# Kernel optimization log

Hardware: AMD Instinct MI355X
Metric: run time of the kernel (lower is better)

## Reference

```python
import jax, jax.numpy as jnp
import numpy as np

ALPHA = 0.2          # LeakyReLU negative slope
NEG = -9e15          # mask fill value, as in pyGAT GraphAttentionLayer
N, NIN, NHID, NOUT = 4096, 64, 32, 64
NHEADS, D_INT = 8, 32
H_INT = max(1, int(NHEADS * 0.25))   # 2 intent heads
H_SP = NHEADS - H_INT                # 6 spatial heads


def setup_inputs() -> dict:
    key = jax.random.key(0)
    ks = jax.random.split(key, 10)
    x = jax.random.normal(ks[0], (N, NIN), dtype=jnp.float32)
    adj = (jax.random.uniform(ks[1], (N, N)) < 0.01).astype(jnp.float32)
    adj = jnp.clip(adj + jnp.eye(N, dtype=jnp.float32), 0.0, 1.0)
    intent_embeds = jax.random.normal(ks[2], (N, D_INT), dtype=jnp.float32)
    # learned params (xavier-ish scale)
    def xav(k, shape):
        fan = shape[-2] if len(shape) > 1 else shape[-1]
        return jax.random.normal(k, shape, dtype=jnp.float32) / np.sqrt(fan)
    W_sp = xav(ks[3], (H_SP, NIN, NHID))       # spatial head projections
    a_sp = xav(ks[4], (H_SP, 2 * NHID))        # spatial attention vectors
    W_int = xav(ks[5], (H_INT, NIN, NHID))     # intent head projections
    a_int = xav(ks[6], (H_INT, 2 * D_INT))     # intent attention vectors (over intent embeds)
    W_out = xav(ks[7], (NHID * NHEADS, NOUT))  # output GAT layer
    a_out = xav(ks[8], (2 * NOUT,))
    return {"x": x, "adj": adj, "intent_embeds": intent_embeds,
            "W_sp": W_sp, "a_sp": a_sp, "W_int": W_int, "a_int": a_int,
            "W_out": W_out, "a_out": a_out}


def _masked_attend(e, mask, Wh):
    # e: [H,N,N] raw scores, mask: [1,N,N] bool, Wh: [H,N,F]
    att = jax.nn.softmax(jnp.where(mask, e, NEG), axis=-1)
    return jnp.einsum('hij,hjf->hif', att, Wh)


def reference(x, adj, intent_embeds, W_sp, a_sp, W_int, a_int, W_out, a_out):
    mask = (adj > 0)[None]                                   # [1,N,N]
    # ---- spatial heads (standard GAT, batched over heads) ----
    Wh_s = jnp.einsum('nf,hfo->hno', x, W_sp)                # [Hs,N,nhid]
    f1 = jnp.einsum('hno,ho->hn', Wh_s, a_sp[:, :NHID])
    f2 = jnp.einsum('hno,ho->hn', Wh_s, a_sp[:, NHID:])
    e_s = jax.nn.leaky_relu(f1[:, :, None] + f2[:, None, :], ALPHA)
    h_s = jax.nn.elu(_masked_attend(e_s, mask, Wh_s))        # concat=True -> elu
    # ---- intent heads: scores from intent embeddings, values from Wh ----
    Wh_i = jnp.einsum('nf,hfo->hno', x, W_int)               # [Hi,N,nhid]
    g1 = jnp.einsum('nd,hd->hn', intent_embeds, a_int[:, :D_INT])
    g2 = jnp.einsum('nd,hd->hn', intent_embeds, a_int[:, D_INT:])
    e_i = jax.nn.leaky_relu(g1[:, :, None] + g2[:, None, :], ALPHA)
    h_i = jax.nn.elu(_masked_attend(e_i, mask, Wh_i))        # [Hi,N,nhid]
    # ---- concat heads along feature dim: [N, nheads*nhid] ----
    h = jnp.concatenate([h_s, h_i], axis=0).transpose(1, 0, 2).reshape(N, -1)
    # ---- output attention layer (concat=False: no elu) ----
    Who = h @ W_out                                          # [N,nout]
    o1 = Who @ a_out[:NOUT]
    o2 = Who @ a_out[NOUT:]
    e_o = jax.nn.leaky_relu(o1[:, None] + o2[None, :], ALPHA)
    att_o = jax.nn.softmax(jnp.where(mask[0], e_o, NEG), axis=-1)
    out = att_o @ Who
    return jnp.tanh(out)
```

## Files before the change

### kernel.cpp

```cpp
#include <hip/hip_runtime.h>

#define N      4096
#define NIN    64
#define NHID   32
#define NOUT   64
#define NHEADS 8
#define H_SP   6
#define D_INT  32
#define MAXDEG 128
#define NPB    4
#define ROWS   8
#define WPAD   (MAXDEG + 4)
#define ALPHA  0.2f

__device__ __forceinline__ int mbcnt64(unsigned long long m) {
    return __builtin_amdgcn_mbcnt_hi((unsigned)(m >> 32),
           __builtin_amdgcn_mbcnt_lo((unsigned)m, 0u));
}

__global__ __launch_bounds__(256) void k_fused1(
    const float* __restrict__ x, const float* __restrict__ ie,
    const float4* __restrict__ adj4,
    const float* __restrict__ Wsp, const float* __restrict__ asp,
    const float* __restrict__ Wint, const float* __restrict__ aint,
    float* __restrict__ Wh_t, float* __restrict__ src, float* __restrict__ dst_t,
    int* __restrict__ col, int* __restrict__ deg)
{
    const int nb   = blockIdx.x * NPB;
    const int tid  = threadIdx.x;
    const int wv   = tid >> 6, lane = tid & 63;
    const int h    = tid >> 5, f    = tid & 31;

    __shared__ float xs_t[NIN][NPB];
    __shared__ float ies[NPB][D_INT];

    xs_t[tid & 63][tid >> 6] = x[nb * NIN + tid];
    if (tid < NPB * D_INT) ies[tid >> 5][tid & 31] = ie[nb * D_INT + tid];
    __syncthreads();

    const float* W = (h < H_SP) ? (Wsp + h * NIN * NHID)
                                : (Wint + (h - H_SP) * NIN * NHID);
    float acc[NPB] = {0.f, 0.f, 0.f, 0.f};
#pragma unroll
    for (int c = 0; c < NIN; ++c) {
        const float wval = W[c * NHID + f];
        const float4 xv  = *(const float4*)&xs_t[c][0];
        acc[0] += xv.x * wval; acc[1] += xv.y * wval;
        acc[2] += xv.z * wval; acc[3] += xv.w * wval;
    }
#pragma unroll
    for (int m = 0; m < NPB; ++m)
        Wh_t[(size_t)(nb + m) * 256 + tid] = acc[m];

    const float a1v = (h < H_SP) ? asp[h * 64 + f]      : aint[(h - H_SP) * 64 + f];
    const float a2v = (h < H_SP) ? asp[h * 64 + 32 + f] : aint[(h - H_SP) * 64 + 32 + f];
#pragma unroll
    for (int m = 0; m < NPB; ++m) {
        const float b = (h < H_SP) ? acc[m] : ies[m][f];
        float s1 = b * a1v, s2 = b * a2v;
#pragma unroll
        for (int mm = 16; mm >= 1; mm >>= 1) {
            s1 += __shfl_xor(s1, mm);
            s2 += __shfl_xor(s2, mm);
        }
        if (f == 0) { src[h * N + nb + m] = s1; dst_t[(nb + m) * 8 + h] = s2; }
    }

    const int r = nb + wv;
    const float4* row = adj4 + (size_t)r * (N / 4);
    int cnt = 0;
#pragma unroll 4
    for (int t = 0; t < 16; ++t) {
        float4 v = row[t * 64 + lane];
        unsigned long long bx = __ballot(v.x > 0.f);
        unsigned long long by = __ballot(v.y > 0.f);
        unsigned long long bz = __ballot(v.z > 0.f);
        unsigned long long bw = __ballot(v.w > 0.f);
        const int tx = __popcll(bx), ty = __popcll(by);
        const int tz = __popcll(bz), tw = __popcll(bw);
        const int idx0 = (t * 64 + lane) * 4;
        const int px = cnt + mbcnt64(bx);
        const int py = cnt + tx + mbcnt64(by);
        const int pz = cnt + tx + ty + mbcnt64(bz);
        const int pw = cnt + tx + ty + tz + mbcnt64(bw);
        if (v.x > 0.f && px < MAXDEG) col[r * MAXDEG + px] = idx0;
        if (v.y > 0.f && py < MAXDEG) col[r * MAXDEG + py] = idx0 + 1;
        if (v.z > 0.f && pz < MAXDEG) col[r * MAXDEG + pz] = idx0 + 2;
        if (v.w > 0.f && pw < MAXDEG) col[r * MAXDEG + pw] = idx0 + 3;
        cnt += tx + ty + tz + tw;
    }
    if (lane == 0) deg[r] = (cnt < MAXDEG) ? cnt : MAXDEG;
}

__global__ __launch_bounds__(512, 4) void k_attn1who(
    const int* __restrict__ col, const int* __restrict__ deg,
    const float* __restrict__ Wh_t, const float* __restrict__ src,
    const float* __restrict__ dst_t, const float* __restrict__ Wout,
    const float* __restrict__ aout,
    float* __restrict__ Who, float* __restrict__ o1, float* __restrict__ o2)
{
    const int r0   = blockIdx.x * ROWS;
    const int tid  = threadIdx.x;
    const int wv   = tid >> 6, lane = tid & 63;
    const int r    = r0 + wv;

    __shared__ __align__(16) int   cs[ROWS][MAXDEG];
    __shared__ __align__(16) float w_t[ROWS][NHEADS][WPAD];
    __shared__ __align__(16) float hs[ROWS][NHEADS * NHID];

    const int d  = deg[r];
    const int j0 = (lane < d)      ? col[r * MAXDEG + lane]      : 0;
    const int j1 = (lane + 64 < d) ? col[r * MAXDEG + 64 + lane] : 0;
    cs[wv][lane]      = j0;
    cs[wv][lane + 64] = j1;

    float sr[NHEADS];
#pragma unroll
    for (int h = 0; h < NHEADS; ++h) sr[h] = src[h * N + r];

    float dA[NHEADS] = {}, dB[NHEADS] = {};
    if (lane < d) {
        *(float4*)&dA[0] = *(const float4*)&dst_t[j0 * 8];
        *(float4*)&dA[4] = *(const float4*)&dst_t[j0 * 8 + 4];
    }
    if (lane + 64 < d) {
        *(float4*)&dB[0] = *(const float4*)&dst_t[j1 * 8];
        *(float4*)&dB[4] = *(const float4*)&dst_t[j1 * 8 + 4];
    }

#pragma unroll
    for (int h = 0; h < NHEADS; ++h) {
        float a = sr[h] + dA[h]; a = a > 0.f ? a : ALPHA * a;
        float b = sr[h] + dB[h]; b = b > 0.f ? b : ALPHA * b;
        w_t[wv][h][lane]      = (lane < d)      ? __expf(a) : 0.f;
        w_t[wv][h][lane + 64] = (lane + 64 < d) ? __expf(b) : 0.f;
    }

    const float* wrow = &w_t[wv][lane >> 3][0];
    const int*   csr_ = &cs[wv][0];
    float4 acc = make_float4(0.f, 0.f, 0.f, 0.f);
    float  ws  = 0.f;
    const int d4 = (d + 3) & ~3;
    for (int k = 0; k < d4; k += 4) {
        const int4   jj = *(const int4*)&csr_[k];
        const float4 wq = *(const float4*)&wrow[k];
        const float4 ga = *(const float4*)&Wh_t[(size_t)jj.x * 256 + 4 * lane];
        const float4 gb = *(const float4*)&Wh_t[(size_t)jj.y * 256 + 4 * lane];
        const float4 gc = *(const float4*)&Wh_t[(size_t)jj.z * 256 + 4 * lane];
        const float4 gd = *(const float4*)&Wh_t[(size_t)jj.w * 256 + 4 * lane];
        ws    += (wq.x + wq.y) + (wq.z + wq.w);
        acc.x += wq.x * ga.x + wq.y * gb.x + wq.z * gc.x + wq.w * gd.x;
        acc.y += wq.x * ga.y + wq.y * gb.y + wq.z * gc.y + wq.w * gd.y;
        acc.z += wq.x * ga.z + wq.y * gb.z + wq.z * gc.z + wq.w * gd.z;
        acc.w += wq.x * ga.w + wq.y * gb.w + wq.z * gc.w + wq.w * gd.w;
    }
    const float inv = 1.f / ws;
    acc.x *= inv; acc.y *= inv; acc.z *= inv; acc.w *= inv;
    acc.x = acc.x > 0.f ? acc.x : __expf(acc.x) - 1.f;
    acc.y = acc.y > 0.f ? acc.y : __expf(acc.y) - 1.f;
    acc.z = acc.z > 0.f ? acc.z : __expf(acc.z) - 1.f;
    acc.w = acc.w > 0.f ? acc.w : __expf(acc.w) - 1.f;
    *(float4*)&hs[wv][4 * lane] = acc;
    __syncthreads();

    float* part = &w_t[0][0][0];
    {
        float wreg[32];
#pragma unroll
        for (int cc = 0; cc < 32; ++cc)
            wreg[cc] = Wout[(wv * 32 + cc) * NOUT + lane];
#pragma unroll
        for (int m = 0; m < ROWS; ++m) {
            float a = 0.f;
#pragma unroll
            for (int cc = 0; cc < 32; cc += 4) {
                const float4 hv = *(const float4*)&hs[m][wv * 32 + cc];
                a += hv.x * wreg[cc]     + hv.y * wreg[cc + 1]
                   + hv.z * wreg[cc + 2] + hv.w * wreg[cc + 3];
            }
            part[(wv * ROWS + m) * NOUT + lane] = a;
        }
    }
    __syncthreads();

    float who = 0.f;
#pragma unroll
    for (int q = 0; q < 8; ++q) who += part[(q * ROWS + wv) * NOUT + lane];
    Who[(size_t)r * NOUT + lane] = who;
    float v1 = who * aout[lane];
    float v2 = who * aout[NOUT + lane];
#pragma unroll
    for (int m = 32; m >= 1; m >>= 1) {
        v1 += __shfl_xor(v1, m);
        v2 += __shfl_xor(v2, m);
    }
    if (lane == 0) { o1[r] = v1; o2[r] = v2; }
}

__global__ __launch_bounds__(256) void k_attn2(
    const int* __restrict__ col, const int* __restrict__ deg,
    const float* __restrict__ Who, const float* __restrict__ o1,
    const float* __restrict__ o2, float* __restrict__ out)
{
    const int tid  = threadIdx.x;
    const int wv   = tid >> 6, lane = tid & 63;
    const int r    = blockIdx.x * 4 + wv;

    const int d  = deg[r];
    const int j0 = (lane < d)      ? col[r * MAXDEG + lane]      : 0;
    const int j1 = (lane + 64 < d) ? col[r * MAXDEG + 64 + lane] : 0;
    const float sr = o1[r];

    float p0 = 0.f, p1 = 0.f;
    if (lane < d) {
        float e = sr + o2[j0]; e = e > 0.f ? e : ALPHA * e;
        p0 = __expf(e);
    }
    if (lane + 64 < d) {
        float e = sr + o2[j1]; e = e > 0.f ? e : ALPHA * e;
        p1 = __expf(e);
    }

    const int sub = lane >> 4, q = lane & 15;
    float4 acc = make_float4(0.f, 0.f, 0.f, 0.f);
    float  sw  = 0.f;
    const int dlo  = d < 64 ? d : 64;
    const int d4a  = (dlo + 3) & ~3;
#pragma unroll 2
    for (int k = 0; k < d4a; k += 4) {
        const int   jj = __shfl(j0, k + sub);
        const float ww = __shfl(p0, k + sub);
        const float4 g = *(const float4*)&Who[(size_t)jj * NOUT + 4 * q];
        sw    += ww;
        acc.x += ww * g.x; acc.y += ww * g.y;
        acc.z += ww * g.z; acc.w += ww * g.w;
    }
    const int d4b = (d + 3) & ~3;
    for (int k = 64; k < d4b; k += 4) {
        const int   jj = __shfl(j1, (k - 64) + sub);
        const float ww = __shfl(p1, (k - 64) + sub);
        const float4 g = *(const float4*)&Who[(size_t)jj * NOUT + 4 * q];
        sw    += ww;
        acc.x += ww * g.x; acc.y += ww * g.y;
        acc.z += ww * g.z; acc.w += ww * g.w;
    }
#pragma unroll
    for (int m = 16; m <= 32; m <<= 1) {
        acc.x += __shfl_xor(acc.x, m);
        acc.y += __shfl_xor(acc.y, m);
        acc.z += __shfl_xor(acc.z, m);
        acc.w += __shfl_xor(acc.w, m);
        sw    += __shfl_xor(sw,    m);
    }
    if (lane < 16) {
        const float inv = 1.f / sw;
        float4 o;
        o.x = tanhf(acc.x * inv); o.y = tanhf(acc.y * inv);
        o.z = tanhf(acc.z * inv); o.w = tanhf(acc.w * inv);
        *(float4*)&out[(size_t)r * NOUT + 4 * lane] = o;
    }
}

extern "C" void kernel_launch(void* const* d_in, const int* in_sizes, int n_in,
                              void* d_out, int out_size, void* d_ws, size_t ws_size,
                              hipStream_t stream) {
    const float* x    = (const float*)d_in[0];
    const float* adj  = (const float*)d_in[1];
    const float* ie   = (const float*)d_in[2];
    const float* Wsp  = (const float*)d_in[3];
    const float* asp  = (const float*)d_in[4];
    const float* Wint = (const float*)d_in[5];
    const float* aint = (const float*)d_in[6];
    const float* Wout = (const float*)d_in[7];
    const float* aout = (const float*)d_in[8];
    float* out = (float*)d_out;

    float* ws    = (float*)d_ws;
    float* Wh_t  = ws;
    float* src   = Wh_t + 1048576;
    float* dst_t = src  + 32768;
    float* Who   = dst_t + 32768;
    float* o1    = Who  + 262144;
    float* o2    = o1   + 4096;
    int*   col   = (int*)(o2 + 4096);
    int*   deg   = col + 4096 * MAXDEG;

    k_fused1  <<<N / NPB,  256, 0, stream>>>(x, ie, (const float4*)adj, Wsp, asp,
                                             Wint, aint, Wh_t, src, dst_t, col, deg);
    k_attn1who<<<N / ROWS, 512, 0, stream>>>(col, deg, Wh_t, src, dst_t, Wout, aout,
                                             Who, o1, o2);
    k_attn2   <<<N / 4,    256, 0, stream>>>(col, deg, Who, o1, o2, out);
}
```

Before: 141.3 us.

## Fuse output attention into attn1 kernel via grid-wide atomic barrier

Merges the output-layer attention kernel into the preceding attention+Who kernel, so there is one fewer launch. A software grid barrier (atomic counter reset by the first kernel, then a spin-wait) makes sure all Who and o2 values are written before the neighbour gather. Each wave reuses its row's already-loaded neighbour indices, degree and o1 value held in registers. The barrier relies on all 512 blocks being co-resident, which should hold given the launch bounds on a large GPU. It adds spin-wait and fence overhead, and there is a deadlock risk if occupancy is lower than assumed.

```diff
diff --git a/kernel.cpp b/kernel.cpp
--- a/kernel.cpp
+++ b/kernel.cpp
@@ -10,6 +10,7 @@
 #define MAXDEG 128
 #define NPB    4
 #define ROWS   8
+#define NBLK2  (N / ROWS)
 #define WPAD   (MAXDEG + 4)
 #define ALPHA  0.2f
 
@@ -24,12 +25,14 @@
     const float* __restrict__ Wsp, const float* __restrict__ asp,
     const float* __restrict__ Wint, const float* __restrict__ aint,
     float* __restrict__ Wh_t, float* __restrict__ src, float* __restrict__ dst_t,
-    int* __restrict__ col, int* __restrict__ deg)
+    int* __restrict__ col, int* __restrict__ deg, int* bar)
 {
     const int nb   = blockIdx.x * NPB;
     const int tid  = threadIdx.x;
     const int wv   = tid >> 6, lane = tid & 63;
     const int h    = tid >> 5, f    = tid & 31;
+
+    if (blockIdx.x == 0 && tid == 0) *bar = 0;
 
     __shared__ float xs_t[NIN][NPB];
     __shared__ float ies[NPB][D_INT];
@@ -92,12 +95,13 @@
     if (lane == 0) deg[r] = (cnt < MAXDEG) ? cnt : MAXDEG;
 }
 
-__global__ __launch_bounds__(512, 4) void k_attn1who(
+__global__ __launch_bounds__(512, 4) void k_attn1who23(
     const int* __restrict__ col, const int* __restrict__ deg,
     const float* __restrict__ Wh_t, const float* __restrict__ src,
     const float* __restrict__ dst_t, const float* __restrict__ Wout,
     const float* __restrict__ aout,
-    float* __restrict__ Who, float* __restrict__ o1, float* __restrict__ o2)
+    float* __restrict__ Who, float* __restrict__ o2,
+    float* __restrict__ out, int* bar)
 {
     const int r0   = blockIdx.x * ROWS;
     const int tid  = threadIdx.x;
@@ -154,8 +158,8 @@
         acc.z += wq.x * ga.z + wq.y * gb.z + wq.z * gc.z + wq.w * gd.z;
         acc.w += wq.x * ga.w + wq.y * gb.w + wq.z * gc.w + wq.w * gd.w;
     }
-    const float inv = 1.f / ws;
-    acc.x *= inv; acc.y *= inv; acc.z *= inv; acc.w *= inv;
+    const float winv = 1.f / ws;
+    acc.x *= winv; acc.y *= winv; acc.z *= winv; acc.w *= winv;
     acc.x = acc.x > 0.f ? acc.x : __expf(acc.x) - 1.f;
     acc.y = acc.y > 0.f ? acc.y : __expf(acc.y) - 1.f;
     acc.z = acc.z > 0.f ? acc.z : __expf(acc.z) - 1.f;
@@ -185,7 +189,7 @@
 
     float who = 0.f;
 #pragma unroll
-    for (int q = 0; q < 8; ++q) who += part[(q * ROWS + wv) * NOUT + lane];
+    for (int q8 = 0; q8 < 8; ++q8) who += part[(q8 * ROWS + wv) * NOUT + lane];
     Who[(size_t)r * NOUT + lane] = who;
     float v1 = who * aout[lane];
     float v2 = who * aout[NOUT + lane];
@@ -194,46 +198,43 @@
         v1 += __shfl_xor(v1, m);
         v2 += __shfl_xor(v2, m);
     }
-    if (lane == 0) { o1[r] = v1; o2[r] = v2; }
-}
-
-__global__ __launch_bounds__(256) void k_attn2(
-    const int* __restrict__ col, const int* __restrict__ deg,
-    const float* __restrict__ Who, const float* __restrict__ o1,
-    const float* __restrict__ o2, float* __restrict__ out)
-{
-    const int tid  = threadIdx.x;
-    const int wv   = tid >> 6, lane = tid & 63;
-    const int r    = blockIdx.x * 4 + wv;
-
-    const int d  = deg[r];
-    const int j0 = (lane < d)      ? col[r * MAXDEG + lane]      : 0;
-    const int j1 = (lane + 64 < d) ? col[r * MAXDEG + 64 + lane] : 0;
-    const float sr = o1[r];
-
+    if (lane == 0) o2[r] = v2;
+
+    __threadfence();
+    __syncthreads();
+    if (tid == 0) {
+        __hip_atomic_fetch_add(bar, 1, __ATOMIC_RELEASE, __HIP_MEMORY_SCOPE_AGENT);
+        int guard = 0;
+        while (__hip_atomic_load(bar, __ATOMIC_ACQUIRE, __HIP_MEMORY_SCOPE_AGENT)
+                   < NBLK2 && ++guard < (1 << 30)) {}
+    }
+    __syncthreads();
+    __threadfence();
+
+    const float sro = v1;
     float p0 = 0.f, p1 = 0.f;
     if (lane < d) {
-        float e = sr + o2[j0]; e = e > 0.f ? e : ALPHA * e;
+        float e = sro + o2[j0]; e = e > 0.f ? e : ALPHA * e;
         p0 = __expf(e);
     }
     if (lane + 64 < d) {
-        float e = sr + o2[j1]; e = e > 0.f ? e : ALPHA * e;
+        float e = sro + o2[j1]; e = e > 0.f ? e : ALPHA * e;
         p1 = __expf(e);
     }
 
     const int sub = lane >> 4, q = lane & 15;
-    float4 acc = make_float4(0.f, 0.f, 0.f, 0.f);
+    float4 oac = make_float4(0.f, 0.f, 0.f, 0.f);
     float  sw  = 0.f;
-    const int dlo  = d < 64 ? d : 64;
-    const int d4a  = (dlo + 3) & ~3;
+    const int dlo = d < 64 ? d : 64;
+    const int d4a = (dlo + 3) & ~3;
 #pragma unroll 2
     for (int k = 0; k < d4a; k += 4) {
         const int   jj = __shfl(j0, k + sub);
         const float ww = __shfl(p0, k + sub);
         const float4 g = *(const float4*)&Who[(size_t)jj * NOUT + 4 * q];
         sw    += ww;
-        acc.x += ww * g.x; acc.y += ww * g.y;
-        acc.z += ww * g.z; acc.w += ww * g.w;
+        oac.x += ww * g.x; oac.y += ww * g.y;
+        oac.z += ww * g.z; oac.w += ww * g.w;
     }
     const int d4b = (d + 3) & ~3;
     for (int k = 64; k < d4b; k += 4) {
@@ -241,22 +242,22 @@
         const float ww = __shfl(p1, (k - 64) + sub);
         const float4 g = *(const float4*)&Who[(size_t)jj * NOUT + 4 * q];
         sw    += ww;
-        acc.x += ww * g.x; acc.y += ww * g.y;
-        acc.z += ww * g.z; acc.w += ww * g.w;
+        oac.x += ww * g.x; oac.y += ww * g.y;
+        oac.z += ww * g.z; oac.w += ww * g.w;
     }
 #pragma unroll
     for (int m = 16; m <= 32; m <<= 1) {
-        acc.x += __shfl_xor(acc.x, m);
-        acc.y += __shfl_xor(acc.y, m);
-        acc.z += __shfl_xor(acc.z, m);
-        acc.w += __shfl_xor(acc.w, m);
+        oac.x += __shfl_xor(oac.x, m);
+        oac.y += __shfl_xor(oac.y, m);
+        oac.z += __shfl_xor(oac.z, m);
+        oac.w += __shfl_xor(oac.w, m);
         sw    += __shfl_xor(sw,    m);
     }
     if (lane < 16) {
         const float inv = 1.f / sw;
         float4 o;
-        o.x = tanhf(acc.x * inv); o.y = tanhf(acc.y * inv);
-        o.z = tanhf(acc.z * inv); o.w = tanhf(acc.w * inv);
+        o.x = tanhf(oac.x * inv); o.y = tanhf(oac.y * inv);
+        o.z = tanhf(oac.z * inv); o.w = tanhf(oac.w * inv);
         *(float4*)&out[(size_t)r * NOUT + 4 * lane] = o;
     }
 }
@@ -284,10 +285,11 @@
     float* o2    = o1   + 4096;
     int*   col   = (int*)(o2 + 4096);
     int*   deg   = col + 4096 * MAXDEG;
-
-    k_fused1  <<<N / NPB,  256, 0, stream>>>(x, ie, (const float4*)adj, Wsp, asp,
-                                             Wint, aint, Wh_t, src, dst_t, col, deg);
-    k_attn1who<<<N / ROWS, 512, 0, stream>>>(col, deg, Wh_t, src, dst_t, Wout, aout,
-                                             Who, o1, o2);
-    k_attn2   <<<N / 4,    256, 0, stream>>>(col, deg, Who, o1, o2, out);
-}
+    int*   bar   = deg + 4096;
+
+    k_fused1    <<<N / NPB, 256, 0, stream>>>(x, ie, (const float4*)adj, Wsp, asp,
+                                              Wint, aint, Wh_t, src, dst_t, col,
+                                              deg, bar);
+    k_attn1who23<<<NBLK2,   512, 0, stream>>>(col, deg, Wh_t, src, dst_t, Wout,
+                                              aout, Who, o2, out, bar);
+}
```

Result: slower. 294.3 us (+108.3%).
